# Optimization experiments

Measured on AMD Instinct MI355X. Metric: run time of the kernel, lower is better.

Reference implementation:

```python
import jax, jax.numpy as jnp
import numpy as np

EPS = 1e-8


def _cross2(a, b):
    return a[..., 0] * b[..., 1] - a[..., 1] * b[..., 0]


def _box2corners(b5):
    # b5: [N,5] = (x, y, w, l, alpha) -> corners [N,4,2], counter-clockwise
    local = jnp.array([[-0.5, -0.5], [0.5, -0.5], [0.5, 0.5], [-0.5, 0.5]], dtype=b5.dtype)
    scaled = local[None, :, :] * b5[:, None, 2:4]            # [N,4,2]
    c, s = jnp.cos(b5[:, 4]), jnp.sin(b5[:, 4])
    x = scaled[..., 0] * c[:, None] - scaled[..., 1] * s[:, None]
    y = scaled[..., 0] * s[:, None] + scaled[..., 1] * c[:, None]
    return jnp.stack([x, y], -1) + b5[:, None, 0:2]


def _corners_in_box(pts, b5):
    # pts: [N,4,2] points, b5: [N,5] boxes -> bool [N,4]
    d = pts - b5[:, None, 0:2]
    c, s = jnp.cos(b5[:, 4])[:, None], jnp.sin(b5[:, 4])[:, None]
    lx = d[..., 0] * c + d[..., 1] * s
    ly = -d[..., 0] * s + d[..., 1] * c
    return (jnp.abs(lx) <= b5[:, None, 2] * 0.5) & (jnp.abs(ly) <= b5[:, None, 3] * 0.5)


def _rotated_intersection_area(b1, b2):
    # b1, b2: [N,5] BEV boxes -> intersection area [N]
    c1, c2 = _box2corners(b1), _box2corners(b2)          # [N,4,2]
    # 16 edge-pair intersections
    p1 = c1[:, :, None, :]                               # [N,4,1,2]
    p2 = jnp.roll(c1, -1, axis=1)[:, :, None, :]
    q1 = c2[:, None, :, :]                               # [N,1,4,2]
    q2 = jnp.roll(c2, -1, axis=1)[:, None, :, :]
    d1, d2 = p2 - p1, q2 - q1
    den = _cross2(d1, d2)                                # [N,4,4]
    ok_den = jnp.abs(den) > EPS
    safe_den = jnp.where(ok_den, den, 1.0)
    t = _cross2(q1 - p1, d2) / safe_den
    s = _cross2(q1 - p1, d1) / safe_den
    valid_e = ok_den & (t >= 0) & (t <= 1) & (s >= 0) & (s <= 1)
    pts_e = jnp.where(valid_e[..., None], p1 + t[..., None] * d1, 0.0)
    N = b1.shape[0]
    pts_e = pts_e.reshape(N, 16, 2)
    valid_e = valid_e.reshape(N, 16)
    # corners of one box inside the other
    in12 = _corners_in_box(c1, b2)                       # [N,4]
    in21 = _corners_in_box(c2, b1)
    verts = jnp.concatenate([pts_e, c1, c2], axis=1)     # [N,24,2]
    mask = jnp.concatenate([valid_e, in12, in21], axis=1)  # [N,24]
    nv = mask.sum(-1)
    centroid = (verts * mask[..., None]).sum(1) / jnp.clip(nv, 1)[:, None]
    rel = verts - centroid[:, None, :]
    rel = jnp.where(mask[..., None], rel, jnp.array([1.0, 0.0], dtype=verts.dtype))
    ang = jnp.where(mask, jnp.arctan2(rel[..., 1], rel[..., 0]), 1e6)
    idx = jnp.argsort(ang, axis=-1)                      # valid verts first, CCW order
    sv = jnp.take_along_axis(verts, idx[..., None], axis=1)
    sm = jnp.take_along_axis(mask, idx, axis=1)
    poly = jnp.where(sm[..., None], sv, sv[:, :1, :])    # pad with first vertex (zero area terms)
    nxt = jnp.roll(poly, -1, axis=1)
    area = 0.5 * jnp.abs(_cross2(poly, nxt).sum(-1))
    return jnp.where(nv >= 3, area, 0.0)


def _cal_iou_3d(b1, b2):
    # b1, b2: [N,7] = (x, y, z, w, h, l, yaw); BEV dims [0,1,3,4,6], height dim 5
    bev1 = b1[:, jnp.array([0, 1, 3, 4, 6])]
    bev2 = b2[:, jnp.array([0, 1, 3, 4, 6])]
    zmax1, zmin1 = b1[:, 2] + 0.5 * b1[:, 5], b1[:, 2] - 0.5 * b1[:, 5]
    zmax2, zmin2 = b2[:, 2] + 0.5 * b2[:, 5], b2[:, 2] - 0.5 * b2[:, 5]
    z_overlap = jnp.clip(jnp.minimum(zmax1, zmax2) - jnp.maximum(zmin1, zmin2), 0.0)
    inter_2d = _rotated_intersection_area(bev1, bev2)
    inter_3d = inter_2d * z_overlap
    v1 = b1[:, 3] * b1[:, 4] * b1[:, 5]
    v2 = b2[:, 3] * b2[:, 4] * b2[:, 5]
    return inter_3d / jnp.clip(v1 + v2 - inter_3d, EPS)


def setup_inputs() -> dict:
    key = jax.random.key(0)
    k1, k2, k3 = jax.random.split(key, 3)
    N = 262144
    r = jax.random.uniform(k1, (N, 7), dtype=jnp.float32)
    xyz = (r[:, :3] - 0.5) * 20.0
    whl = r[:, 3:6] * 2.0 + 0.5
    yaw = (r[:, 6:7] - 0.5) * np.pi
    pred = jnp.concatenate([xyz, whl, yaw], axis=-1)
    # target = pred + small perturbation so IoU is nontrivial
    dp = jax.random.uniform(k2, (N, 7), dtype=jnp.float32) - 0.5
    target = pred + dp * jnp.array([0.4, 0.4, 0.4, 0.3, 0.3, 0.3, 0.4], dtype=jnp.float32)
    target = target.at[:, 3:6].set(jnp.clip(target[:, 3:6], 0.1))
    weight = jax.random.uniform(k3, (N,), dtype=jnp.float32)
    return {"pred": pred, "target": target, "weight": weight}


def reference(pred, target, weight):
    # IoU3DLoss(with_yaw=True, reduction='mean', loss_weight=1.0)
    loss = 1.0 - _cal_iou_3d(pred, target)   # [N]
    loss = loss * weight
    return 1.0 * loss.mean()
```

## Files before the change

### kernel.cpp

```cpp
#include <hip/hip_runtime.h>
#include <math.h>

#define IEPS 1e-8f
#define BIGF 3.0e38f

typedef float f4 __attribute__((ext_vector_type(4)));
struct __attribute__((packed, aligned(4))) F4u { f4 v; };

__device__ __forceinline__ float fast_rcp(float x) { return __builtin_amdgcn_rcpf(x); }

__device__ __forceinline__ float slab_dt(float px, float py, float dx, float dy,
                                         float hw, float hh)
{
    float rdx = fast_rcp(dx), rdy = fast_rcp(dy);
    float ax = (-hw - px) * rdx, bx = (hw - px) * rdx;
    float ay = (-hh - py) * rdy, by = (hh - py) * rdy;
    float txmin = fminf(ax, bx), txmax = fmaxf(ax, bx);
    float tymin = fminf(ay, by), tymax = fmaxf(ay, by);
    if (dx == 0.0f) { bool in = fabsf(px) <= hw; txmin = in ? -BIGF : BIGF; txmax = in ? BIGF : -BIGF; }
    if (dy == 0.0f) { bool in = fabsf(py) <= hh; tymin = in ? -BIGF : BIGF; tymax = in ? BIGF : -BIGF; }
    float t0 = fmaxf(fmaxf(txmin, tymin), 0.0f);
    float t1 = fminf(fminf(txmax, tymax), 1.0f);
    return fmaxf(t1 - t0, 0.0f);
}

__global__ __launch_bounds__(256) void iou3d_partial_kernel(
    const float* __restrict__ pred,
    const float* __restrict__ target,
    const float* __restrict__ weight,
    float* __restrict__ partial,
    int N)
{
    int i = blockIdx.x * blockDim.x + threadIdx.x;
    float contrib = 0.0f;

    if (i < N) {
        const float* P = pred + (size_t)i * 7;
        const float* T = target + (size_t)i * 7;
        f4 pA = ((const F4u*)P)->v;
        f4 pB = ((const F4u*)(P + 3))->v;
        f4 tA = ((const F4u*)T)->v;
        f4 tB = ((const F4u*)(T + 3))->v;

        float cx1 = pA[0], cy1 = pA[1], z1 = pA[2];
        float w1 = pA[3], h1 = pB[1], dz1 = pB[2], yaw1 = pB[3];
        float cx2 = tA[0], cy2 = tA[1], z2 = tA[2];
        float w2 = tA[3], h2 = tB[1], dz2 = tB[2], yaw2 = tB[3];

        float hw1 = 0.5f * w1, hh1 = 0.5f * h1;
        float hw2 = 0.5f * w2, hh2 = 0.5f * h2;
        float c1a = __cosf(yaw1), s1a = __sinf(yaw1);
        float c2a = __cosf(yaw2), s2a = __sinf(yaw2);

        float dxg = cx2 - cx1, dyg = cy2 - cy1;
        float t12x =  dxg * c1a + dyg * s1a;
        float t12y = -dxg * s1a + dyg * c1a;
        float t21x = -(dxg * c2a + dyg * s2a);
        float t21y = -(-dxg * s2a + dyg * c2a);
        float cr = c2a * c1a + s2a * s1a;
        float sr = s2a * c1a - c2a * s1a;

        const float sgx[4] = {-1.0f, 1.0f, 1.0f, -1.0f};
        const float sgy[4] = {-1.0f, -1.0f, 1.0f, 1.0f};

        float q1x[4], q1y[4];
        float p2x[4], p2y[4];
        #pragma unroll
        for (int k = 0; k < 4; ++k) {
            float ux = sgx[k] * hw2, uy = sgy[k] * hh2;
            q1x[k] = t12x + ux * cr - uy * sr;
            q1y[k] = t12y + ux * sr + uy * cr;
            float vx = sgx[k] * hw1, vy = sgy[k] * hh1;
            p2x[k] = t21x + vx * cr + vy * sr;
            p2y[k] = t21y - vx * sr + vy * cr;
        }

        float area2 = 0.0f;
        float sum_dt2 = 0.0f;
        #pragma unroll
        for (int k = 0; k < 4; ++k) {
            int k1 = (k + 1) & 3;
            float dx = p2x[k1] - p2x[k], dy = p2y[k1] - p2y[k];
            float dt = slab_dt(p2x[k], p2y[k], dx, dy, hw2, hh2);
            area2 += dt * (p2x[k] * dy - p2y[k] * dx);
            float ex = q1x[k1] - q1x[k], ey = q1y[k1] - q1y[k];
            sum_dt2 += slab_dt(q1x[k], q1y[k], ex, ey, hw1, hh1);
        }
        area2 += 2.0f * hw2 * hh2 * sum_dt2;
        float inter2d = 0.5f * fabsf(area2);

        float hz1 = 0.5f * dz1, hz2 = 0.5f * dz2;
        float zo = fmaxf(fminf(z1 + hz1, z2 + hz2) - fmaxf(z1 - hz1, z2 - hz2), 0.0f);

        float inter3d = inter2d * zo;
        float v1 = w1 * h1 * dz1;
        float v2 = w2 * h2 * dz2;
        float denom = fmaxf(v1 + v2 - inter3d, IEPS);
        float iou = inter3d / denom;

        contrib = weight[i] * (1.0f - iou);
    }

    #pragma unroll
    for (int off = 32; off > 0; off >>= 1)
        contrib += __shfl_down(contrib, off);

    __shared__ float sred[4];
    int lane = threadIdx.x & 63;
    int wid  = threadIdx.x >> 6;
    if (lane == 0) sred[wid] = contrib;
    __syncthreads();
    if (threadIdx.x == 0)
        partial[blockIdx.x] = sred[0] + sred[1] + sred[2] + sred[3];
}

__global__ __launch_bounds__(1024) void iou3d_reduce_kernel(
    const float* __restrict__ partial, float* __restrict__ out,
    int nPart, float invN)
{
    int t = threadIdx.x;
    float s = 0.0f;
    for (int k = t; k < nPart; k += 1024) s += partial[k];

    #pragma unroll
    for (int off = 32; off > 0; off >>= 1)
        s += __shfl_down(s, off);

    __shared__ float sm[16];
    if ((t & 63) == 0) sm[t >> 6] = s;
    __syncthreads();
    if (t == 0) {
        float tot = 0.0f;
        #pragma unroll
        for (int k = 0; k < 16; ++k) tot += sm[k];
        out[0] = tot * invN;
    }
}

extern "C" void kernel_launch(void* const* d_in, const int* in_sizes, int n_in,
                              void* d_out, int out_size, void* d_ws, size_t ws_size,
                              hipStream_t stream) {
    const float* pred   = (const float*)d_in[0];
    const float* target = (const float*)d_in[1];
    const float* weight = (const float*)d_in[2];
    float* out = (float*)d_out;
    float* partial = (float*)d_ws;

    int N = in_sizes[0] / 7;
    float invN = 1.0f / (float)N;

    int block = 256;
    int grid = (N + block - 1) / block;
    iou3d_partial_kernel<<<grid, block, 0, stream>>>(pred, target, weight, partial, N);
    iou3d_reduce_kernel<<<1, 1024, 0, stream>>>(partial, out, grid, invN);
}
```

Measured before the change: 10.89 us.

## Share edge reciprocals across parallel box edges and drop block-level reduction sync

Measured after the change: 14.36 us. 1.32x slower.

```diff
diff --git a/kernel.cpp b/kernel.cpp
--- a/kernel.cpp
+++ b/kernel.cpp
@@ -2,38 +2,34 @@
 #include <math.h>
 
 #define IEPS 1e-8f
-#define BIGF 3.0e38f
 
 typedef float f4 __attribute__((ext_vector_type(4)));
 struct __attribute__((packed, aligned(4))) F4u { f4 v; };
 
 __device__ __forceinline__ float fast_rcp(float x) { return __builtin_amdgcn_rcpf(x); }
 
-__device__ __forceinline__ float slab_dt(float px, float py, float dx, float dy,
+__device__ __forceinline__ float slab_dt(float px, float py, float rdx, float rdy,
                                          float hw, float hh)
 {
-    float rdx = fast_rcp(dx), rdy = fast_rcp(dy);
     float ax = (-hw - px) * rdx, bx = (hw - px) * rdx;
     float ay = (-hh - py) * rdy, by = (hh - py) * rdy;
-    float txmin = fminf(ax, bx), txmax = fmaxf(ax, bx);
-    float tymin = fminf(ay, by), tymax = fmaxf(ay, by);
-    if (dx == 0.0f) { bool in = fabsf(px) <= hw; txmin = in ? -BIGF : BIGF; txmax = in ? BIGF : -BIGF; }
-    if (dy == 0.0f) { bool in = fabsf(py) <= hh; tymin = in ? -BIGF : BIGF; tymax = in ? BIGF : -BIGF; }
-    float t0 = fmaxf(fmaxf(txmin, tymin), 0.0f);
-    float t1 = fminf(fminf(txmax, tymax), 1.0f);
+    float t0 = fmaxf(fmaxf(fminf(ax, bx), fminf(ay, by)), 0.0f);
+    float t1 = fminf(fminf(fmaxf(ax, bx), fmaxf(ay, by)), 1.0f);
     return fmaxf(t1 - t0, 0.0f);
 }
 
-__global__ __launch_bounds__(256) void iou3d_partial_kernel(
+__global__ __launch_bounds__(256, 4) void iou3d_partial_kernel(
     const float* __restrict__ pred,
     const float* __restrict__ target,
     const float* __restrict__ weight,
     float* __restrict__ partial,
     int N)
 {
-    int i = blockIdx.x * blockDim.x + threadIdx.x;
+    const int t   = threadIdx.x;
+    const int bid = blockIdx.x;
+    const int i   = bid * 256 + t;
+
     float contrib = 0.0f;
-
     if (i < N) {
         const float* P = pred + (size_t)i * 7;
         const float* T = target + (size_t)i * 7;
@@ -56,37 +52,44 @@
         float t12x =  dxg * c1a + dyg * s1a;
         float t12y = -dxg * s1a + dyg * c1a;
         float t21x = -(dxg * c2a + dyg * s2a);
-        float t21y = -(-dxg * s2a + dyg * c2a);
+        float t21y =  (dxg * s2a - dyg * c2a);
         float cr = c2a * c1a + s2a * s1a;
         float sr = s2a * c1a - c2a * s1a;
 
-        const float sgx[4] = {-1.0f, 1.0f, 1.0f, -1.0f};
-        const float sgy[4] = {-1.0f, -1.0f, 1.0f, 1.0f};
+        float exx = hw1 * cr, exy = -hw1 * sr;
+        float eyx = hh1 * sr, eyy =  hh1 * cr;
+        float p0x = t21x - exx - eyx, p0y = t21y - exy - eyy;
+        float p1x = t21x + exx - eyx, p1y = t21y + exy - eyy;
+        float p2x = t21x + exx + eyx, p2y = t21y + exy + eyy;
+        float p3x = t21x - exx + eyx, p3y = t21y - exy + eyy;
+        float d0x = exx + exx, d0y = exy + exy;
+        float d1x = eyx + eyx, d1y = eyy + eyy;
+        float rd0x = fast_rcp(d0x), rd0y = fast_rcp(d0y);
+        float rd1x = fast_rcp(d1x), rd1y = fast_rcp(d1y);
 
-        float q1x[4], q1y[4];
-        float p2x[4], p2y[4];
-        #pragma unroll
-        for (int k = 0; k < 4; ++k) {
-            float ux = sgx[k] * hw2, uy = sgy[k] * hh2;
-            q1x[k] = t12x + ux * cr - uy * sr;
-            q1y[k] = t12y + ux * sr + uy * cr;
-            float vx = sgx[k] * hw1, vy = sgy[k] * hh1;
-            p2x[k] = t21x + vx * cr + vy * sr;
-            p2y[k] = t21y - vx * sr + vy * cr;
-        }
+        float area2 = 0.0f, dt;
+        dt = slab_dt(p0x, p0y,  rd0x,  rd0y, hw2, hh2); area2 += dt * (p0x * d0y - p0y * d0x);
+        dt = slab_dt(p1x, p1y,  rd1x,  rd1y, hw2, hh2); area2 += dt * (p1x * d1y - p1y * d1x);
+        dt = slab_dt(p2x, p2y, -rd0x, -rd0y, hw2, hh2); area2 -= dt * (p2x * d0y - p2y * d0x);
+        dt = slab_dt(p3x, p3y, -rd1x, -rd1y, hw2, hh2); area2 -= dt * (p3x * d1y - p3y * d1x);
 
-        float area2 = 0.0f;
-        float sum_dt2 = 0.0f;
-        #pragma unroll
-        for (int k = 0; k < 4; ++k) {
-            int k1 = (k + 1) & 3;
-            float dx = p2x[k1] - p2x[k], dy = p2y[k1] - p2y[k];
-            float dt = slab_dt(p2x[k], p2y[k], dx, dy, hw2, hh2);
-            area2 += dt * (p2x[k] * dy - p2y[k] * dx);
-            float ex = q1x[k1] - q1x[k], ey = q1y[k1] - q1y[k];
-            sum_dt2 += slab_dt(q1x[k], q1y[k], ex, ey, hw1, hh1);
-        }
-        area2 += 2.0f * hw2 * hh2 * sum_dt2;
+        float fxx =  hw2 * cr, fxy = hw2 * sr;
+        float fyx = -hh2 * sr, fyy = hh2 * cr;
+        float q0x = t12x - fxx - fyx, q0y = t12y - fxy - fyy;
+        float q1x = t12x + fxx - fyx, q1y = t12y + fxy - fyy;
+        float q2x = t12x + fxx + fyx, q2y = t12y + fxy + fyy;
+        float q3x = t12x - fxx + fyx, q3y = t12y - fxy + fyy;
+        float g0x = fxx + fxx, g0y = fxy + fxy;
+        float g1x = fyx + fyx, g1y = fyy + fyy;
+        float rg0x = fast_rcp(g0x), rg0y = fast_rcp(g0y);
+        float rg1x = fast_rcp(g1x), rg1y = fast_rcp(g1y);
+
+        float sdt = slab_dt(q0x, q0y,  rg0x,  rg0y, hw1, hh1)
+                  + slab_dt(q1x, q1y,  rg1x,  rg1y, hw1, hh1)
+                  + slab_dt(q2x, q2y, -rg0x, -rg0y, hw1, hh1)
+                  + slab_dt(q3x, q3y, -rg1x, -rg1y, hw1, hh1);
+        area2 += 2.0f * hw2 * hh2 * sdt;
+
         float inter2d = 0.5f * fabsf(area2);
 
         float hz1 = 0.5f * dz1, hz2 = 0.5f * dz2;
@@ -105,36 +108,27 @@
     for (int off = 32; off > 0; off >>= 1)
         contrib += __shfl_down(contrib, off);
 
-    __shared__ float sred[4];
-    int lane = threadIdx.x & 63;
-    int wid  = threadIdx.x >> 6;
-    if (lane == 0) sred[wid] = contrib;
-    __syncthreads();
-    if (threadIdx.x == 0)
-        partial[blockIdx.x] = sred[0] + sred[1] + sred[2] + sred[3];
+    if ((t & 63) == 0)
+        partial[bid * 4 + (t >> 6)] = contrib;
 }
 
-__global__ __launch_bounds__(1024) void iou3d_reduce_kernel(
+__global__ __launch_bounds__(256) void iou3d_reduce_kernel(
     const float* __restrict__ partial, float* __restrict__ out,
     int nPart, float invN)
 {
     int t = threadIdx.x;
     float s = 0.0f;
-    for (int k = t; k < nPart; k += 1024) s += partial[k];
+    for (int k = t; k < nPart; k += 256) s += partial[k];
 
     #pragma unroll
     for (int off = 32; off > 0; off >>= 1)
         s += __shfl_down(s, off);
 
-    __shared__ float sm[16];
+    __shared__ float sm[4];
     if ((t & 63) == 0) sm[t >> 6] = s;
     __syncthreads();
-    if (t == 0) {
-        float tot = 0.0f;
-        #pragma unroll
-        for (int k = 0; k < 16; ++k) tot += sm[k];
-        out[0] = tot * invN;
-    }
+    if (t == 0)
+        out[0] = (sm[0] + sm[1] + sm[2] + sm[3]) * invN;
 }
 
 extern "C" void kernel_launch(void* const* d_in, const int* in_sizes, int n_in,
@@ -152,5 +146,5 @@
     int block = 256;
     int grid = (N + block - 1) / block;
     iou3d_partial_kernel<<<grid, block, 0, stream>>>(pred, target, weight, partial, N);
-    iou3d_reduce_kernel<<<1, 1024, 0, stream>>>(partial, out, grid, invN);
+    iou3d_reduce_kernel<<<1, 256, 0, stream>>>(partial, out, grid * 4, invN);
 }
```
